# Performance work log

Measured on AMD Instinct MI355X. Metric: run time of the kernel, lower is better.

## Reference

```python
import jax, jax.numpy as jnp
import numpy as np

B, T, C = 4, 2048, 1024
H = 16
D = C // H  # 64


def setup_inputs() -> dict:
    key = jax.random.key(0)
    ks = jax.random.split(key, 5)
    scale = 0.02
    x = jax.random.normal(ks[0], (B, T, C), dtype=jnp.float32)
    # Linear weights stored in [in, out] layout (equivalent to torch W.T)
    W_qkv = jax.random.normal(ks[1], (C, 3 * C), dtype=jnp.float32) * scale
    b_qkv = jax.random.normal(ks[2], (3 * C,), dtype=jnp.float32) * scale
    W_out = jax.random.normal(ks[3], (C, C), dtype=jnp.float32) * scale
    b_out = jax.random.normal(ks[4], (C,), dtype=jnp.float32) * scale
    return {"x": x, "W_qkv": W_qkv, "b_qkv": b_qkv, "W_out": W_out, "b_out": b_out}


def reference(x, W_qkv, b_qkv, W_out, b_out):
    Bx, Tx, Cx = x.shape
    qkv = x @ W_qkv + b_qkv                      # [B,T,3C]
    qkv = qkv.reshape(Bx, Tx, 3, H, D)
    q = jnp.transpose(qkv[:, :, 0], (0, 2, 1, 3))  # [B,H,T,D]
    k = jnp.transpose(qkv[:, :, 1], (0, 2, 1, 3))
    v = jnp.transpose(qkv[:, :, 2], (0, 2, 1, 3))
    scores = jnp.einsum('bhqd,bhkd->bhqk', q, k) / jnp.sqrt(jnp.float32(D))
    causal = jnp.tril(jnp.ones((Tx, Tx), dtype=bool))  # keep lower triangle
    scores = jnp.where(causal, scores, jnp.float32(-jnp.inf))
    w = jax.nn.softmax(scores, axis=-1)           # dropout p=0.0 (eval)
    out = jnp.einsum('bhqk,bhkd->bhqd', w, v)     # [B,H,T,D]
    out = jnp.transpose(out, (0, 2, 1, 3)).reshape(Bx, Tx, Cx)
    return out @ W_out + b_out
```

## Files before the change

kernel.cpp:

```cpp
#include <hip/hip_runtime.h>

typedef _Float16 f16;
typedef _Float16 f16x4 __attribute__((ext_vector_type(4)));
typedef _Float16 f16x8 __attribute__((ext_vector_type(8)));
typedef float    f32x4 __attribute__((ext_vector_type(4)));

#define B_ 4
#define T_ 2048
#define C_ 1024
#define H_ 16
#define D_ 64

__device__ __forceinline__ void gload_lds16(const f16* g, f16* l) {
  __builtin_amdgcn_global_load_lds(
      (const __attribute__((address_space(1))) unsigned int*)g,
      (__attribute__((address_space(3))) unsigned int*)l, 16, 0, 0);
}

__global__ void cvt_kernel(const float* __restrict__ in, f16* __restrict__ out, int n4) {
  int i = blockIdx.x * blockDim.x + threadIdx.x;
  int stride = gridDim.x * blockDim.x;
  for (; i < n4; i += stride) {
    float4 v = ((const float4*)in)[i];
    f16x4 h = { (f16)v.x, (f16)v.y, (f16)v.z, (f16)v.w };
    ((f16x4*)out)[i] = h;
  }
}

__global__ void transpose_cvt_kernel(const float* __restrict__ W, f16* __restrict__ Wt,
                                     int K, int N) {
  __shared__ f16 tile[32][33];
  int bx = blockIdx.x, by = blockIdx.y;
  int tx = threadIdx.x & 31, ty = threadIdx.x >> 5;
  #pragma unroll
  for (int i = ty; i < 32; i += 8)
    tile[i][tx] = (f16)W[(size_t)(by * 32 + i) * N + bx * 32 + tx];
  __syncthreads();
  #pragma unroll
  for (int i = ty; i < 32; i += 8)
    Wt[(size_t)(bx * 32 + i) * K + by * 32 + tx] = tile[tx][i];
}

template <int EPI>
__global__ __launch_bounds__(256, 3)
void gemm_kernel(const f16* __restrict__ A, const f16* __restrict__ Bt,
                 const float* __restrict__ bias, float* __restrict__ outF,
                 f16* __restrict__ q, f16* __restrict__ kk, f16* __restrict__ vt,
                 int M, int N, int K) {
  __shared__ __align__(16) f16 As[3][128 * 32];
  __shared__ __align__(16) f16 Bs[3][128 * 32];
  const int nbn = N >> 7;
  const int bid = blockIdx.x;
  const int bm = bid / nbn, bn = bid % nbn;
  const int m0 = bm << 7, n0 = bn << 7;
  const int tid = threadIdx.x;
  const int lane = tid & 63, wid = tid >> 6;
  const int wr = wid >> 1, wc = wid & 1;

  f32x4 acc[4][4] = {};

  const int srow = lane >> 2;
  const int scol = (((lane & 3) ^ ((lane >> 2) & 3)) << 3);
  const f16* Abase = A + (size_t)(m0 + srow) * K + scol;
  const f16* Bbase = Bt + (size_t)(n0 + srow) * K + scol;

  auto stage = [&](int buf, int kt) {
    const int c0 = wid * 2;
    #pragma unroll
    for (int c = c0; c < c0 + 2; ++c) {
      gload_lds16(Abase + (size_t)c * 16 * K + kt * 32, &As[buf][c * 512]);
      gload_lds16(Bbase + (size_t)c * 16 * K + kt * 32, &Bs[buf][c * 512]);
    }
  };

  const int g = lane >> 4;
  const int rr = lane & 15;
  const int swz = (g ^ (rr & 3)) << 4;

  auto compute = [&](int buf) {
    f16x8 af[4], bf[4];
    #pragma unroll
    for (int t = 0; t < 4; ++t) {
      af[t] = *(const f16x8*)((const char*)&As[buf][0] + (wr * 64 + t * 16 + rr) * 64 + swz);
      bf[t] = *(const f16x8*)((const char*)&Bs[buf][0] + (wc * 64 + t * 16 + rr) * 64 + swz);
    }
    __builtin_amdgcn_s_setprio(1);
    #pragma unroll
    for (int i = 0; i < 4; ++i)
      #pragma unroll
      for (int j = 0; j < 4; ++j)
        acc[i][j] = __builtin_amdgcn_mfma_f32_16x16x32_f16(af[i], bf[j], acc[i][j], 0, 0, 0);
    __builtin_amdgcn_s_setprio(0);
  };

  const int nk = K >> 5;
  int bcur = 0, bnext = 1, bnn = 2;
  stage(0, 0);
  stage(1, 1);
  asm volatile("s_waitcnt vmcnt(4)" ::: "memory");
  __builtin_amdgcn_s_barrier();
  __builtin_amdgcn_sched_barrier(0);
  for (int t = 0; t < nk; ++t) {
    if (t + 2 < nk) stage(bnn, t + 2);
    compute(bcur);
    if (t + 1 < nk) {
      if (t + 2 < nk) asm volatile("s_waitcnt vmcnt(4)" ::: "memory");
      else            asm volatile("s_waitcnt vmcnt(0)" ::: "memory");
      __builtin_amdgcn_s_barrier();
      __builtin_amdgcn_sched_barrier(0);
    }
    const int tmp = bcur; bcur = bnext; bnext = bnn; bnn = tmp;
  }

  const int col = lane & 15;
  const int row4 = (lane >> 4) << 2;
  #pragma unroll
  for (int i = 0; i < 4; ++i) {
    #pragma unroll
    for (int j = 0; j < 4; ++j) {
      const int n = n0 + wc * 64 + j * 16 + col;
      const float bn_ = bias[n];
      #pragma unroll
      for (int r = 0; r < 4; ++r) {
        const int m = m0 + wr * 64 + i * 16 + row4 + r;
        const float v = acc[i][j][r] + bn_;
        if (EPI == 1) {
          outF[(size_t)m * N + n] = v;
        } else {
          const int which = n >> 10;
          const int cc = n & 1023;
          const int h = cc >> 6, d = cc & 63;
          const int b = m >> 11, t = m & 2047;
          const size_t bh = (size_t)b * 16 + h;
          const f16 hv = (f16)v;
          if (which == 0)      q [(bh * T_ + t) * D_ + d] = hv;
          else if (which == 1) kk[(bh * T_ + t) * D_ + d] = hv;
          else                 vt[(bh * D_ + d) * T_ + t] = hv;
        }
      }
    }
  }
}

__global__ __launch_bounds__(512, 2)
void attn_kernel(const f16* __restrict__ Q, const f16* __restrict__ Kg,
                 const f16* __restrict__ Vt, f16* __restrict__ Aout) {
  __shared__ __align__(16) f16 Ks[2][64 * 64];
  __shared__ __align__(16) f16 Vs[2][64 * 64];
  __shared__ __align__(16) f16 Pt[8][16][72];

  const int bid = blockIdx.x;
  const int wgid = (bid & 7) * 128 + (bid >> 3);
  const int bh = wgid >> 4;
  const int ti = 15 - (wgid & 15);
  const int lane = threadIdx.x & 63, w = threadIdx.x >> 6;
  const int col = lane & 15;
  const int g = lane >> 4;
  const int ko = g << 3;

  const f16* Qp = Q + (size_t)bh * T_ * D_;
  const f16* Kp = Kg + (size_t)bh * T_ * D_;
  const f16* Vp = Vt + (size_t)bh * D_ * T_;

  const int srow8 = lane >> 3;
  const int scb = ((lane & 7) << 4) ^ (srow8 << 4);
  const int krow_s = (w << 3) + srow8;

  auto stage = [&](int buf, int kb) {
    gload_lds16(Kp + (size_t)(kb + krow_s) * D_ + (scb >> 1), &Ks[buf][w * 512]);
    gload_lds16(Vp + (size_t)krow_s * T_ + kb + (scb >> 1), &Vs[buf][w * 512]);
  };
  auto ldsK = [&](int buf, int krow, int d0) -> f16x8 {
    const int off = krow * 128 + ((d0 << 1) ^ ((krow & 7) << 4));
    return *(const f16x8*)((const char*)&Ks[buf][0] + off);
  };
  auto ldsV = [&](int buf, int drow, int k0) -> f16x8 {
    const int off = drow * 128 + ((k0 << 1) ^ ((drow & 7) << 4));
    return *(const f16x8*)((const char*)&Vs[buf][0] + off);
  };

  const int q0 = ti << 7;
  const int qrow0 = q0 + (w << 4);
  const int nkt = (ti << 1) + 2;
  const int qg = qrow0 + col;

  f16x8 qf[2];
  #pragma unroll
  for (int s = 0; s < 2; ++s) {
    f16x8 t = *(const f16x8*)&Qp[(size_t)qg * D_ + s * 32 + ko];
    #pragma unroll
    for (int e = 0; e < 8; ++e) t[e] = t[e] * (f16)0.125f;
    qf[s] = t;
  }

  f32x4 o[4] = {};
  float m = -1e30f, l = 0.f;

  stage(0, 0);
  __syncthreads();
  int cur = 0;
  for (int kt = 0; kt < nkt; ++kt) {
    const int kb = kt << 6;
    if (kt + 1 < nkt) stage(cur ^ 1, (kt + 1) << 6);

    if (kb <= qrow0 + 15) {
      f32x4 sc[4] = {};
      #pragma unroll
      for (int s = 0; s < 2; ++s)
        #pragma unroll
        for (int mt = 0; mt < 4; ++mt) {
          f16x8 kf = ldsK(cur, mt * 16 + col, s * 32 + ko);
          sc[mt] = __builtin_amdgcn_mfma_f32_16x16x32_f16(kf, qf[s], sc[mt], 0, 0, 0);
        }

      const bool needMask = (kb + 63 > qrow0);
      if (needMask) {
        #pragma unroll
        for (int mt = 0; mt < 4; ++mt)
          #pragma unroll
          for (int r = 0; r < 4; ++r)
            if (kb + mt * 16 + (g << 2) + r > qg) sc[mt][r] = -1e30f;
      }

      float mx = fmaxf(fmaxf(fmaxf(sc[0][0], sc[0][1]), fmaxf(sc[0][2], sc[0][3])),
                       fmaxf(fmaxf(sc[1][0], sc[1][1]), fmaxf(sc[1][2], sc[1][3])));
      mx = fmaxf(mx, fmaxf(fmaxf(fmaxf(sc[2][0], sc[2][1]), fmaxf(sc[2][2], sc[2][3])),
                           fmaxf(fmaxf(sc[3][0], sc[3][1]), fmaxf(sc[3][2], sc[3][3]))));
      mx = fmaxf(mx, __shfl_xor(mx, 16, 64));
      mx = fmaxf(mx, __shfl_xor(mx, 32, 64));

      if (!__all(mx - m <= 8.f)) {
        const float mnew = fmaxf(m, mx);
        const float alpha = __expf(m - mnew);
        m = mnew;
        l *= alpha;
        #pragma unroll
        for (int mt = 0; mt < 4; ++mt)
          #pragma unroll
          for (int r = 0; r < 4; ++r) o[mt][r] *= alpha;
      }

      float rs = 0.f;
      #pragma unroll
      for (int mt = 0; mt < 4; ++mt) {
        f16x4 ph;
        #pragma unroll
        for (int r = 0; r < 4; ++r) {
          const float p = __expf(sc[mt][r] - m);
          rs += p;
          ph[r] = (f16)p;
        }
        *(f16x4*)&Pt[w][col][mt * 16 + (g << 2)] = ph;
      }
      rs += __shfl_xor(rs, 16, 64);
      rs += __shfl_xor(rs, 32, 64);
      l += rs;

      #pragma unroll
      for (int s = 0; s < 2; ++s) {
        f16x8 pb = *(const f16x8*)&Pt[w][col][s * 32 + ko];
        #pragma unroll
        for (int mt = 0; mt < 4; ++mt) {
          f16x8 vf = ldsV(cur, mt * 16 + col, s * 32 + ko);
          o[mt] = __builtin_amdgcn_mfma_f32_16x16x32_f16(vf, pb, o[mt], 0, 0, 0);
        }
      }
    }

    __syncthreads();
    cur ^= 1;
  }

  const int b = bh >> 4, h = bh & 15;
  const float inv = 1.0f / l;
  const size_t rowoff = ((size_t)b * T_ + qg) * C_ + (size_t)h * D_;
  #pragma unroll
  for (int mt = 0; mt < 4; ++mt) {
    f16x4 ov;
    #pragma unroll
    for (int r = 0; r < 4; ++r) ov[r] = (f16)(o[mt][r] * inv);
    *(f16x4*)&Aout[rowoff + mt * 16 + (g << 2)] = ov;
  }
}

extern "C" void kernel_launch(void* const* d_in, const int* in_sizes, int n_in,
                              void* d_out, int out_size, void* d_ws, size_t ws_size,
                              hipStream_t stream) {
  const float* x    = (const float*)d_in[0];
  const float* Wqkv = (const float*)d_in[1];
  const float* bqkv = (const float*)d_in[2];
  const float* Wout = (const float*)d_in[3];
  const float* bout = (const float*)d_in[4];
  float* out = (float*)d_out;

  char* ws = (char*)d_ws;
  f16* xb     = (f16*)ws;
  f16* Wqkv_t = (f16*)(ws + (16u << 20));
  f16* Wout_t = (f16*)(ws + (22u << 20));
  f16* Qb     = (f16*)(ws + (24u << 20));
  f16* Kb     = (f16*)(ws + (40u << 20));
  f16* Vtb    = (f16*)(ws + (56u << 20));

  cvt_kernel<<<2048, 256, 0, stream>>>(x, xb, (B_ * T_ * C_) / 4);
  dim3 g1(3072 / 32, 1024 / 32);
  transpose_cvt_kernel<<<g1, 256, 0, stream>>>(Wqkv, Wqkv_t, 1024, 3072);
  dim3 g2(1024 / 32, 1024 / 32);
  transpose_cvt_kernel<<<g2, 256, 0, stream>>>(Wout, Wout_t, 1024, 1024);

  gemm_kernel<0><<<64 * 24, 256, 0, stream>>>(xb, Wqkv_t, bqkv, nullptr,
                                              Qb, Kb, Vtb, 8192, 3072, 1024);
  attn_kernel<<<1024, 512, 0, stream>>>(Qb, Kb, Vtb, xb );
  gemm_kernel<1><<<64 * 8, 256, 0, stream>>>(xb, Wout_t, bout, out,
                                             nullptr, nullptr, nullptr, 8192, 1024, 1024);
}
```

Measured before the change: 227.7 us.

## Add 256x256 tiled QKV GEMM kernel with interleaved double-buffered staging

Replaces the QKV projection GEMM with a dedicated 512-thread kernel using 256x256 output tiles, 64-wide K tiles, fine-grained interleaving of global-to-LDS loads with MFMA blocks, and an XCD-aware block remapping. Larger tiles raise arithmetic intensity and cut global traffic per FLOP. The generic GEMM loses its templated epilogue and also drops its LDS swizzle, which risks bank conflicts in the output projection. 384 blocks on the device may leave a partial wave tail.

```diff
diff --git a/kernel.cpp b/kernel.cpp
--- a/kernel.cpp
+++ b/kernel.cpp
@@ -41,11 +41,147 @@
     Wt[(size_t)(bx * 32 + i) * K + by * 32 + tx] = tile[tx][i];
 }
 
-template <int EPI>
+__global__ __launch_bounds__(512, 2)
+void gemm256_kernel(const f16* __restrict__ A, const f16* __restrict__ Bt,
+                    const float* __restrict__ bias,
+                    f16* __restrict__ q, f16* __restrict__ kk, f16* __restrict__ vt) {
+  const int M_ = 8192, N_ = 3072, K_ = 1024;
+  __shared__ __align__(16) f16 As[2][2][128 * 64];
+  __shared__ __align__(16) f16 Bs[2][2][128 * 64];
+
+  const int bid = blockIdx.x;
+  const int wg = (bid & 7) * 48 + (bid >> 3);
+  const int bm = wg / 12, bn = wg % 12;
+  const int m0 = bm << 8, n0 = bn << 8;
+  const int lane = threadIdx.x & 63, wid = threadIdx.x >> 6;
+  const int wm = wid >> 2;
+  const int bhalf = (wid >> 1) & 1;
+  const int brow0 = (wid & 1) << 6;
+  const int rr = lane & 15, g = lane >> 4;
+  const int swz = (rr & 4) << 3;
+
+  f32x4 acc[8][4] = {};
+
+  const int srow = (wid << 3) + (lane >> 3);
+  const int scol = ((((lane & 7) << 4) ^ (lane & 32)) >> 1);
+  const f16* Abase = A + (size_t)(m0 + srow) * K_ + scol;
+  const f16* Bbase = Bt + (size_t)(n0 + srow) * K_ + scol;
+
+  auto STAGE_A = [&](int buf, int half, int tile) {
+    #pragma unroll
+    for (int c = 0; c < 2; ++c)
+      gload_lds16(Abase + (size_t)(half * 128 + c * 64) * K_ + tile * 64,
+                  &As[buf][half][c * 4096 + wid * 512]);
+  };
+  auto STAGE_B = [&](int buf, int half, int tile) {
+    #pragma unroll
+    for (int c = 0; c < 2; ++c)
+      gload_lds16(Bbase + (size_t)(half * 128 + c * 64) * K_ + tile * 64,
+                  &Bs[buf][half][c * 4096 + wid * 512]);
+  };
+
+  auto LDA = [&](int buf, int mhalf, int kkk, f16x8* af) {
+    #pragma unroll
+    for (int f = 0; f < 4; ++f)
+      af[f] = *(const f16x8*)((const char*)&As[buf][wm][0]
+               + (mhalf * 64 + f * 16 + rr) * 128 + ((kkk * 64 + g * 16) ^ swz));
+  };
+  auto LDB = [&](int buf, int kkk, f16x8* bf) {
+    #pragma unroll
+    for (int nf = 0; nf < 4; ++nf)
+      bf[nf] = *(const f16x8*)((const char*)&Bs[buf][bhalf][0]
+               + (brow0 + nf * 16 + rr) * 128 + ((kkk * 64 + g * 16) ^ swz));
+  };
+
+  #define BAR() { __builtin_amdgcn_s_barrier(); __builtin_amdgcn_sched_barrier(0); }
+  #define MMA(MH, AF, BF) { \
+    __builtin_amdgcn_s_setprio(1); \
+    _Pragma("unroll") \
+    for (int f = 0; f < 4; ++f) \
+      _Pragma("unroll") \
+      for (int nf = 0; nf < 4; ++nf) \
+        acc[(MH) * 4 + f][nf] = \
+            __builtin_amdgcn_mfma_f32_16x16x32_f16(AF[f], BF[nf], acc[(MH) * 4 + f][nf], 0, 0, 0); \
+    __builtin_amdgcn_s_setprio(0); }
+
+  STAGE_A(0, 0, 0); STAGE_A(0, 1, 0);
+  STAGE_B(0, 0, 0); STAGE_B(0, 1, 0);
+  STAGE_B(1, 0, 1);
+  asm volatile("s_waitcnt vmcnt(2)" ::: "memory");
+  BAR();
+
+  const int NT = 16;
+  #pragma unroll 1
+  for (int i = 0; i < 8; ++i) {
+    const int t1 = 2 * i + 1, t2 = 2 * i + 2, t3 = 2 * i + 3;
+    f16x8 af[4], bf[4];
+    LDB(0, 0, bf); LDA(0, 0, 0, af);
+    STAGE_B(1, 1, t1);
+    BAR(); MMA(0, af, bf); BAR();
+    LDA(0, 1, 0, af);
+    STAGE_A(1, 0, t1);
+    BAR(); MMA(1, af, bf); BAR();
+    LDB(0, 1, bf); LDA(0, 0, 1, af);
+    STAGE_A(1, 1, t1);
+    BAR(); MMA(0, af, bf); BAR();
+    LDA(0, 1, 1, af);
+    if (t2 < NT) {
+      STAGE_B(0, 0, t2);
+      asm volatile("s_waitcnt vmcnt(2)" ::: "memory");
+    } else {
+      asm volatile("s_waitcnt vmcnt(0)" ::: "memory");
+    }
+    BAR(); MMA(1, af, bf); BAR();
+    LDB(1, 0, bf); LDA(1, 0, 0, af);
+    if (t2 < NT) STAGE_B(0, 1, t2);
+    BAR(); MMA(0, af, bf); BAR();
+    LDA(1, 1, 0, af);
+    if (t2 < NT) STAGE_A(0, 0, t2);
+    BAR(); MMA(1, af, bf); BAR();
+    LDB(1, 1, bf); LDA(1, 0, 1, af);
+    if (t2 < NT) STAGE_A(0, 1, t2);
+    BAR(); MMA(0, af, bf); BAR();
+    LDA(1, 1, 1, af);
+    if (t3 < NT) {
+      STAGE_B(1, 0, t3);
+      asm volatile("s_waitcnt vmcnt(2)" ::: "memory");
+    } else if (i < 7) {
+      asm volatile("s_waitcnt vmcnt(0)" ::: "memory");
+    }
+    BAR(); MMA(1, af, bf); BAR();
+  }
+  #undef MMA
+  #undef BAR
+
+  const int col = lane & 15;
+  const int row4 = (lane >> 4) << 2;
+  const int seg = n0 >> 10;
+  #pragma unroll
+  for (int mi = 0; mi < 8; ++mi) {
+    #pragma unroll
+    for (int nf = 0; nf < 4; ++nf) {
+      const int n = n0 + (wid & 3) * 64 + nf * 16 + col;
+      const float bn_ = bias[n];
+      const int cc = n & 1023;
+      const int h = cc >> 6, d = cc & 63;
+      #pragma unroll
+      for (int r = 0; r < 4; ++r) {
+        const int m = m0 + wm * 128 + mi * 16 + row4 + r;
+        const float v = acc[mi][nf][r] + bn_;
+        const int b = m >> 11, t = m & 2047;
+        const size_t bh = (size_t)b * 16 + h;
+        const f16 hv = (f16)v;
+        if (seg == 0)      q [(bh * T_ + t) * D_ + d] = hv;
+        else if (seg == 1) kk[(bh * T_ + t) * D_ + d] = hv;
+        else               vt[(bh * D_ + d) * T_ + t] = hv;
+      }
+    }
+  }
+}
+
 __global__ __launch_bounds__(256, 3)
 void gemm_kernel(const f16* __restrict__ A, const f16* __restrict__ Bt,
                  const float* __restrict__ bias, float* __restrict__ outF,
-                 f16* __restrict__ q, f16* __restrict__ kk, f16* __restrict__ vt,
                  int M, int N, int K) {
   __shared__ __align__(16) f16 As[3][128 * 32];
   __shared__ __align__(16) f16 Bs[3][128 * 32];
@@ -60,7 +196,7 @@
   f32x4 acc[4][4] = {};
 
   const int srow = lane >> 2;
-  const int scol = (((lane & 3) ^ ((lane >> 2) & 3)) << 3);
+  const int scol = (lane & 3) << 3;
   const f16* Abase = A + (size_t)(m0 + srow) * K + scol;
   const f16* Bbase = Bt + (size_t)(n0 + srow) * K + scol;
 
@@ -73,16 +209,15 @@
     }
   };
 
-  const int g = lane >> 4;
+  const int ko = (lane >> 4) << 3;
   const int rr = lane & 15;
-  const int swz = (g ^ (rr & 3)) << 4;
 
   auto compute = [&](int buf) {
     f16x8 af[4], bf[4];
     #pragma unroll
     for (int t = 0; t < 4; ++t) {
-      af[t] = *(const f16x8*)((const char*)&As[buf][0] + (wr * 64 + t * 16 + rr) * 64 + swz);
-      bf[t] = *(const f16x8*)((const char*)&Bs[buf][0] + (wc * 64 + t * 16 + rr) * 64 + swz);
+      af[t] = *(const f16x8*)&As[buf][(wr * 64 + t * 16 + rr) * 32 + ko];
+      bf[t] = *(const f16x8*)&Bs[buf][(wc * 64 + t * 16 + rr) * 32 + ko];
     }
     __builtin_amdgcn_s_setprio(1);
     #pragma unroll
@@ -123,20 +258,7 @@
       #pragma unroll
       for (int r = 0; r < 4; ++r) {
         const int m = m0 + wr * 64 + i * 16 + row4 + r;
-        const float v = acc[i][j][r] + bn_;
-        if (EPI == 1) {
-          outF[(size_t)m * N + n] = v;
-        } else {
-          const int which = n >> 10;
-          const int cc = n & 1023;
-          const int h = cc >> 6, d = cc & 63;
-          const int b = m >> 11, t = m & 2047;
-          const size_t bh = (size_t)b * 16 + h;
-          const f16 hv = (f16)v;
-          if (which == 0)      q [(bh * T_ + t) * D_ + d] = hv;
-          else if (which == 1) kk[(bh * T_ + t) * D_ + d] = hv;
-          else                 vt[(bh * D_ + d) * T_ + t] = hv;
-        }
+        outF[(size_t)m * N + n] = acc[i][j][r] + bn_;
       }
     }
   }
@@ -307,9 +429,7 @@
   dim3 g2(1024 / 32, 1024 / 32);
   transpose_cvt_kernel<<<g2, 256, 0, stream>>>(Wout, Wout_t, 1024, 1024);
 
-  gemm_kernel<0><<<64 * 24, 256, 0, stream>>>(xb, Wqkv_t, bqkv, nullptr,
-                                              Qb, Kb, Vtb, 8192, 3072, 1024);
+  gemm256_kernel<<<384, 512, 0, stream>>>(xb, Wqkv_t, bqkv, Qb, Kb, Vtb);
   attn_kernel<<<1024, 512, 0, stream>>>(Qb, Kb, Vtb, xb );
-  gemm_kernel<1><<<64 * 8, 256, 0, stream>>>(xb, Wout_t, bout, out,
-                                             nullptr, nullptr, nullptr, 8192, 1024, 1024);
-}
+  gemm_kernel<<<64 * 8, 256, 0, stream>>>(xb, Wout_t, bout, out, 8192, 1024, 1024);
+}
```

Result: no change. 229.2 us (+0.7%).

## Enlarge attention query tile to 256 rows with paired causal tiles and triple buffering

Applied to the files above, without the earlier changes.

Each attention workgroup now processes 256 query rows, with 32 rows per wave, so every K/V fragment loaded from LDS feeds two MFMA streams. Each block handles a complementary pair of causal tiles (ti and 7-ti) to balance work, and the grid shrinks to 256 blocks. K/V staging moves to a three-buffer ring with explicit vmcnt waits and raw barriers. The aim is less LDS and global traffic per unit of work, at the cost of more registers, occupancy limited to one block per SIMD set, and only 256 blocks to fill the GPU.

```diff
diff --git a/kernel.cpp b/kernel.cpp
--- a/kernel.cpp
+++ b/kernel.cpp
@@ -142,17 +142,17 @@
   }
 }
 
-__global__ __launch_bounds__(512, 2)
+__global__ __launch_bounds__(512, 1)
 void attn_kernel(const f16* __restrict__ Q, const f16* __restrict__ Kg,
                  const f16* __restrict__ Vt, f16* __restrict__ Aout) {
-  __shared__ __align__(16) f16 Ks[2][64 * 64];
-  __shared__ __align__(16) f16 Vs[2][64 * 64];
-  __shared__ __align__(16) f16 Pt[8][16][72];
+  __shared__ __align__(16) f16 Ks[3][64 * 64];
+  __shared__ __align__(16) f16 Vs[3][64 * 64];
+  __shared__ __align__(16) f16 Pt[8][32][72];
 
   const int bid = blockIdx.x;
-  const int wgid = (bid & 7) * 128 + (bid >> 3);
-  const int bh = wgid >> 4;
-  const int ti = 15 - (wgid & 15);
+  const int wgid = (bid & 7) * 32 + (bid >> 3);
+  const int bh = wgid >> 2;
+  const int pair = wgid & 3;
   const int lane = threadIdx.x & 63, w = threadIdx.x >> 6;
   const int col = lane & 15;
   const int g = lane >> 4;
@@ -179,107 +179,142 @@
     return *(const f16x8*)((const char*)&Vs[buf][0] + off);
   };
 
-  const int q0 = ti << 7;
-  const int qrow0 = q0 + (w << 4);
-  const int nkt = (ti << 1) + 2;
-  const int qg = qrow0 + col;
-
-  f16x8 qf[2];
-  #pragma unroll
-  for (int s = 0; s < 2; ++s) {
-    f16x8 t = *(const f16x8*)&Qp[(size_t)qg * D_ + s * 32 + ko];
-    #pragma unroll
-    for (int e = 0; e < 8; ++e) t[e] = t[e] * (f16)0.125f;
-    qf[s] = t;
-  }
-
-  f32x4 o[4] = {};
-  float m = -1e30f, l = 0.f;
-
-  stage(0, 0);
-  __syncthreads();
-  int cur = 0;
-  for (int kt = 0; kt < nkt; ++kt) {
-    const int kb = kt << 6;
-    if (kt + 1 < nkt) stage(cur ^ 1, (kt + 1) << 6);
-
-    if (kb <= qrow0 + 15) {
-      f32x4 sc[4] = {};
+  const int b = bh >> 4, hd = bh & 15;
+
+  #pragma unroll 1
+  for (int tt = 0; tt < 2; ++tt) {
+    const int ti = tt ? (7 - pair) : pair;
+    const int q0 = ti << 8;
+    const int qrow0 = q0 + (w << 5);
+    const int nkt = (ti + 1) << 2;
+
+    f16x8 qf[2][2];
+    #pragma unroll
+    for (int h = 0; h < 2; ++h)
       #pragma unroll
-      for (int s = 0; s < 2; ++s)
-        #pragma unroll
-        for (int mt = 0; mt < 4; ++mt) {
-          f16x8 kf = ldsK(cur, mt * 16 + col, s * 32 + ko);
-          sc[mt] = __builtin_amdgcn_mfma_f32_16x16x32_f16(kf, qf[s], sc[mt], 0, 0, 0);
-        }
-
-      const bool needMask = (kb + 63 > qrow0);
-      if (needMask) {
-        #pragma unroll
-        for (int mt = 0; mt < 4; ++mt)
-          #pragma unroll
-          for (int r = 0; r < 4; ++r)
-            if (kb + mt * 16 + (g << 2) + r > qg) sc[mt][r] = -1e30f;
+      for (int s = 0; s < 2; ++s) {
+        f16x8 t = *(const f16x8*)&Qp[(size_t)(qrow0 + h * 16 + col) * D_ + s * 32 + ko];
+        #pragma unroll
+        for (int e = 0; e < 8; ++e) t[e] = t[e] * (f16)0.125f;
+        qf[h][s] = t;
       }
 
-      float mx = fmaxf(fmaxf(fmaxf(sc[0][0], sc[0][1]), fmaxf(sc[0][2], sc[0][3])),
-                       fmaxf(fmaxf(sc[1][0], sc[1][1]), fmaxf(sc[1][2], sc[1][3])));
-      mx = fmaxf(mx, fmaxf(fmaxf(fmaxf(sc[2][0], sc[2][1]), fmaxf(sc[2][2], sc[2][3])),
-                           fmaxf(fmaxf(sc[3][0], sc[3][1]), fmaxf(sc[3][2], sc[3][3]))));
-      mx = fmaxf(mx, __shfl_xor(mx, 16, 64));
-      mx = fmaxf(mx, __shfl_xor(mx, 32, 64));
-
-      if (!__all(mx - m <= 8.f)) {
-        const float mnew = fmaxf(m, mx);
-        const float alpha = __expf(m - mnew);
-        m = mnew;
-        l *= alpha;
-        #pragma unroll
-        for (int mt = 0; mt < 4; ++mt)
-          #pragma unroll
-          for (int r = 0; r < 4; ++r) o[mt][r] *= alpha;
+    f32x4 o[2][4] = {};
+    float m[2] = {-1e30f, -1e30f}, l[2] = {0.f, 0.f};
+
+    int b0 = 0, b1 = 1, b2 = 2;
+    stage(b0, 0);
+    stage(b1, 64);
+    asm volatile("s_waitcnt vmcnt(2)" ::: "memory");
+    __builtin_amdgcn_s_barrier();
+    __builtin_amdgcn_sched_barrier(0);
+
+    for (int kt = 0; kt < nkt; ++kt) {
+      const int kb = kt << 6;
+      if (kt + 2 < nkt) stage(b2, kb + 128);
+
+      if (kb <= qrow0 + 31) {
+        f32x4 sc[2][4] = {};
+        #pragma unroll
+        for (int s = 0; s < 2; ++s)
+          #pragma unroll
+          for (int mt = 0; mt < 4; ++mt) {
+            f16x8 kf = ldsK(b0, mt * 16 + col, s * 32 + ko);
+            sc[0][mt] = __builtin_amdgcn_mfma_f32_16x16x32_f16(kf, qf[0][s], sc[0][mt], 0, 0, 0);
+            sc[1][mt] = __builtin_amdgcn_mfma_f32_16x16x32_f16(kf, qf[1][s], sc[1][mt], 0, 0, 0);
+          }
+
+        if (kb + 63 > qrow0) {
+          #pragma unroll
+          for (int mt = 0; mt < 4; ++mt)
+            #pragma unroll
+            for (int r = 0; r < 4; ++r) {
+              const int kv = kb + mt * 16 + (g << 2) + r;
+              if (kv > qrow0 + col)      sc[0][mt][r] = -1e30f;
+              if (kv > qrow0 + 16 + col) sc[1][mt][r] = -1e30f;
+            }
+        }
+
+        float mx[2];
+        #pragma unroll
+        for (int h = 0; h < 2; ++h) {
+          float v = fmaxf(fmaxf(fmaxf(sc[h][0][0], sc[h][0][1]), fmaxf(sc[h][0][2], sc[h][0][3])),
+                          fmaxf(fmaxf(sc[h][1][0], sc[h][1][1]), fmaxf(sc[h][1][2], sc[h][1][3])));
+          v = fmaxf(v, fmaxf(fmaxf(fmaxf(sc[h][2][0], sc[h][2][1]), fmaxf(sc[h][2][2], sc[h][2][3])),
+                             fmaxf(fmaxf(sc[h][3][0], sc[h][3][1]), fmaxf(sc[h][3][2], sc[h][3][3]))));
+          v = fmaxf(v, __shfl_xor(v, 16, 64));
+          v = fmaxf(v, __shfl_xor(v, 32, 64));
+          mx[h] = v;
+        }
+
+        if (!__all(fmaxf(mx[0] - m[0], mx[1] - m[1]) <= 8.f)) {
+          #pragma unroll
+          for (int h = 0; h < 2; ++h) {
+            const float mnew = fmaxf(m[h], mx[h]);
+            const float alpha = __expf(m[h] - mnew);
+            m[h] = mnew;
+            l[h] *= alpha;
+            #pragma unroll
+            for (int mt = 0; mt < 4; ++mt)
+              #pragma unroll
+              for (int r = 0; r < 4; ++r) o[h][mt][r] *= alpha;
+          }
+        }
+
+        #pragma unroll
+        for (int h = 0; h < 2; ++h) {
+          float rs = 0.f;
+          #pragma unroll
+          for (int mt = 0; mt < 4; ++mt) {
+            f16x4 ph;
+            #pragma unroll
+            for (int r = 0; r < 4; ++r) {
+              const float p = __expf(sc[h][mt][r] - m[h]);
+              rs += p;
+              ph[r] = (f16)p;
+            }
+            *(f16x4*)&Pt[w][h * 16 + col][mt * 16 + (g << 2)] = ph;
+          }
+          rs += __shfl_xor(rs, 16, 64);
+          rs += __shfl_xor(rs, 32, 64);
+          l[h] += rs;
+        }
+
+        #pragma unroll
+        for (int s = 0; s < 2; ++s) {
+          f16x8 pb0 = *(const f16x8*)&Pt[w][col][s * 32 + ko];
+          f16x8 pb1 = *(const f16x8*)&Pt[w][16 + col][s * 32 + ko];
+          #pragma unroll
+          for (int mt = 0; mt < 4; ++mt) {
+            f16x8 vf = ldsV(b0, mt * 16 + col, s * 32 + ko);
+            o[0][mt] = __builtin_amdgcn_mfma_f32_16x16x32_f16(vf, pb0, o[0][mt], 0, 0, 0);
+            o[1][mt] = __builtin_amdgcn_mfma_f32_16x16x32_f16(vf, pb1, o[1][mt], 0, 0, 0);
+          }
+        }
       }
 
-      float rs = 0.f;
+      __builtin_amdgcn_sched_barrier(0);
+      if (kt + 2 < nkt) asm volatile("s_waitcnt vmcnt(2)" ::: "memory");
+      else              asm volatile("s_waitcnt vmcnt(0)" ::: "memory");
+      __builtin_amdgcn_s_barrier();
+      __builtin_amdgcn_sched_barrier(0);
+      const int tmp = b0; b0 = b1; b1 = b2; b2 = tmp;
+    }
+
+    #pragma unroll
+    for (int h = 0; h < 2; ++h) {
+      const float inv = 1.0f / l[h];
+      const int t = qrow0 + h * 16 + col;
+      const size_t rowoff = ((size_t)b * T_ + t) * C_ + (size_t)hd * D_;
       #pragma unroll
       for (int mt = 0; mt < 4; ++mt) {
-        f16x4 ph;
-        #pragma unroll
-        for (int r = 0; r < 4; ++r) {
-          const float p = __expf(sc[mt][r] - m);
-          rs += p;
-          ph[r] = (f16)p;
-        }
-        *(f16x4*)&Pt[w][col][mt * 16 + (g << 2)] = ph;
+        f16x4 ov;
+        #pragma unroll
+        for (int r = 0; r < 4; ++r) ov[r] = (f16)(o[h][mt][r] * inv);
+        *(f16x4*)&Aout[rowoff + mt * 16 + (g << 2)] = ov;
       }
-      rs += __shfl_xor(rs, 16, 64);
-      rs += __shfl_xor(rs, 32, 64);
-      l += rs;
-
-      #pragma unroll
-      for (int s = 0; s < 2; ++s) {
-        f16x8 pb = *(const f16x8*)&Pt[w][col][s * 32 + ko];
-        #pragma unroll
-        for (int mt = 0; mt < 4; ++mt) {
-          f16x8 vf = ldsV(cur, mt * 16 + col, s * 32 + ko);
-          o[mt] = __builtin_amdgcn_mfma_f32_16x16x32_f16(vf, pb, o[mt], 0, 0, 0);
-        }
-      }
-    }
-
-    __syncthreads();
-    cur ^= 1;
-  }
-
-  const int b = bh >> 4, h = bh & 15;
-  const float inv = 1.0f / l;
-  const size_t rowoff = ((size_t)b * T_ + qg) * C_ + (size_t)h * D_;
-  #pragma unroll
-  for (int mt = 0; mt < 4; ++mt) {
-    f16x4 ov;
-    #pragma unroll
-    for (int r = 0; r < 4; ++r) ov[r] = (f16)(o[mt][r] * inv);
-    *(f16x4*)&Aout[rowoff + mt * 16 + (g << 2)] = ov;
+    }
+    __builtin_amdgcn_s_barrier();
   }
 }
 
@@ -309,7 +344,7 @@
 
   gemm_kernel<0><<<64 * 24, 256, 0, stream>>>(xb, Wqkv_t, bqkv, nullptr,
                                               Qb, Kb, Vtb, 8192, 3072, 1024);
-  attn_kernel<<<1024, 512, 0, stream>>>(Qb, Kb, Vtb, xb );
+  attn_kernel<<<256, 512, 0, stream>>>(Qb, Kb, Vtb, xb );
   gemm_kernel<1><<<64 * 8, 256, 0, stream>>>(xb, Wout_t, bout, out,
                                              nullptr, nullptr, nullptr, 8192, 1024, 1024);
 }
```

Result: faster. 213.1 us (-6.4%).
